# Performance work log

Measured on AMD Instinct MI355X. Metric: run time of the kernel, lower is better.

## Reference

```python
import jax, jax.numpy as jnp
import numpy as np

B, S, D = 2, 2048, 1024
H = 16
HD = D // H


def setup_inputs() -> dict:
    key = jax.random.key(0)
    ks = jax.random.split(key, 6)
    x = jax.random.normal(ks[0], (B, S, D), dtype=jnp.float32)
    scale = 1.0 / np.sqrt(D)
    Wq = jax.random.normal(ks[1], (D, D), dtype=jnp.float32) * scale
    Wk = jax.random.normal(ks[2], (D, D), dtype=jnp.float32) * scale
    Wv = jax.random.normal(ks[3], (D, D), dtype=jnp.float32) * scale
    Wo = jax.random.normal(ks[4], (D, D), dtype=jnp.float32) * scale
    bo = jax.random.normal(ks[5], (D,), dtype=jnp.float32) * 0.01
    return {"x": x, "Wq": Wq, "Wk": Wk, "Wv": Wv, "Wo": Wo, "bo": bo}


def reference(x, Wq, Wk, Wv, Wo, bo):
    b, t, _ = x.shape
    # QKV projections (no bias), split into heads: [b, h, t, hd]
    q = (x @ Wq).reshape(b, t, H, HD).transpose(0, 2, 1, 3)
    k = (x @ Wk).reshape(b, t, H, HD).transpose(0, 2, 1, 3)
    v = (x @ Wv).reshape(b, t, H, HD).transpose(0, 2, 1, 3)
    # scores [b, h, t, t]; causal mask (upper triangle -> -inf) applied before scaling
    scores = jnp.einsum("bhqd,bhkd->bhqk", q, k)
    causal = jnp.triu(jnp.ones((t, t), dtype=bool), k=1)
    scores = jnp.where(causal, -jnp.inf, scores)
    attn = jax.nn.softmax(scores / jnp.sqrt(jnp.asarray(HD, scores.dtype)), axis=-1)
    ctx = jnp.einsum("bhqk,bhkd->bhqd", attn, v)
    ctx = ctx.transpose(0, 2, 1, 3).reshape(b, t, H * HD)
    return ctx @ Wo + bo
```

## Files before the change

### kernel.cpp

```cpp
#include <hip/hip_runtime.h>

#define B_ 2
#define S_ 2048
#define D_ 1024
#define H_ 16
#define HD_ 64
#define M_ (B_*S_)

typedef __attribute__((ext_vector_type(8))) short bf16x8;
typedef __attribute__((ext_vector_type(4))) short s16x4;
typedef __attribute__((ext_vector_type(4))) float f32x4;
typedef __attribute__((ext_vector_type(4))) unsigned int u32x4;

static __device__ __forceinline__ unsigned short f2bf(float f) {
  unsigned int u = __builtin_bit_cast(unsigned int, f);
  u += 0x7FFFu + ((u >> 16) & 1u);
  return (unsigned short)(u >> 16);
}

static __device__ __forceinline__ unsigned int cvt_pk_bf16(float a, float b) {
  unsigned int r;
  asm("v_cvt_pk_bf16_f32 %0, %1, %2" : "=v"(r) : "v"(a), "v"(b));
  return r;
}

static __device__ __forceinline__ void gload_lds16(const void* g, void* l) {
  __builtin_amdgcn_global_load_lds(
      (const __attribute__((address_space(1))) unsigned int*)g,
      (__attribute__((address_space(3))) unsigned int*)l, 16, 0, 0);
}

__global__ __launch_bounds__(256) void xcvt_kernel(const float* __restrict__ x,
                                                   unsigned short* __restrict__ xb) {
  size_t i = ((size_t)blockIdx.x * 256 + threadIdx.x) * 8;
  float4 a = ((const float4*)(x + i))[0];
  float4 b = ((const float4*)(x + i))[1];
  bf16x8 w;
  w[0]=(short)f2bf(a.x); w[1]=(short)f2bf(a.y); w[2]=(short)f2bf(a.z); w[3]=(short)f2bf(a.w);
  w[4]=(short)f2bf(b.x); w[5]=(short)f2bf(b.y); w[6]=(short)f2bf(b.z); w[7]=(short)f2bf(b.w);
  *(bf16x8*)(xb + i) = w;
}

__global__ void wtrans_kernel(const float* __restrict__ Wq, const float* __restrict__ Wk,
                              const float* __restrict__ Wv, const float* __restrict__ Wo,
                              unsigned short* __restrict__ wt) {
  __shared__ float tile[32][33];
  const float* W = blockIdx.z==0 ? Wq : blockIdx.z==1 ? Wk : blockIdx.z==2 ? Wv : Wo;
  unsigned short* out = wt + (size_t)blockIdx.z * D_ * D_;
  int n0 = blockIdx.x*32, k0 = blockIdx.y*32;
  int tx = threadIdx.x, ty = threadIdx.y;
  #pragma unroll
  for (int i=0;i<4;i++) tile[ty+i*8][tx] = W[(size_t)(k0+ty+i*8)*D_ + n0+tx];
  __syncthreads();
  #pragma unroll
  for (int i=0;i<4;i++) out[(size_t)(n0+ty+i*8)*D_ + (k0+tx)] = f2bf(tile[tx][ty+i*8]);
}

#define GEMM_K_LOOP(Abase, Bbase)                                                     \
  for (int ks = 0; ks < 16; ++ks) {                                                   \
    const int k0 = ks * 64;                                                           \
    __syncthreads();                                                                  \
    _Pragma("unroll")                                                                 \
    for (int p = 0; p < 4; ++p) {                                                     \
      int c = p*256 + t;                                                              \
      int row = c >> 3, sl = (c & 7) ^ (row & 7);                                     \
      gload_lds16(Abase + (size_t)row*D_ + k0 + sl*8, &As[(p*256 + wid*64)*8]);       \
    }                                                                                 \
    _Pragma("unroll")                                                                 \
    for (int p = 0; p < 4; ++p) {                                                     \
      int c = p*256 + t;                                                              \
      int row = c >> 3, sl = (c & 7) ^ (row & 7);                                     \
      gload_lds16(Bbase + (size_t)row*D_ + k0 + sl*8, &Bs[(p*256 + wid*64)*8]);       \
    }                                                                                 \
    __syncthreads();                                                                  \
    _Pragma("unroll")                                                                 \
    for (int kk = 0; kk < 2; ++kk) {                                                  \
      bf16x8 af[4], bfr[4];                                                           \
      _Pragma("unroll")                                                               \
      for (int m = 0; m < 4; ++m) {                                                   \
        int row = wr + m*16 + l15;                                                    \
        af[m] = *(const bf16x8*)((const char*)As + row*128 + (((kk*4+lg)^(row&7))<<4)); \
      }                                                                               \
      _Pragma("unroll")                                                               \
      for (int n = 0; n < 4; ++n) {                                                   \
        int row = wc + n*16 + l15;                                                    \
        bfr[n] = *(const bf16x8*)((const char*)Bs + row*128 + (((kk*4+lg)^(row&7))<<4)); \
      }                                                                               \
      _Pragma("unroll")                                                               \
      for (int m = 0; m < 4; ++m)                                                     \
        _Pragma("unroll")                                                             \
        for (int n = 0; n < 4; ++n)                                                   \
          acc[m][n] = __builtin_amdgcn_mfma_f32_16x16x32_bf16(af[m], bfr[n], acc[m][n], 0,0,0); \
    }                                                                                 \
  }

__global__ __launch_bounds__(256,3) void gemm_qkv_kernel(
    const unsigned short* __restrict__ xb, const unsigned short* __restrict__ wt,
    unsigned short* __restrict__ Qo, unsigned short* __restrict__ Ko,
    unsigned short* __restrict__ Vto) {
  __shared__ __align__(16) unsigned short As[128*64];
  __shared__ __align__(16) unsigned short Bs[128*64];
  const int z = blockIdx.z;
  const int m0 = blockIdx.y*128, n0 = blockIdx.x*128;
  const int t = threadIdx.x, lane = t & 63, wid = t >> 6;
  const int wr = (wid>>1)*64, wc = (wid&1)*64;
  const int l15 = lane & 15, lg = lane >> 4;
  const unsigned short* Ab = xb + (size_t)m0 * D_;
  const unsigned short* Bb = wt + (size_t)z * D_ * D_ + (size_t)n0 * D_;

  f32x4 acc[4][4];
  #pragma unroll
  for (int m=0;m<4;m++)
    #pragma unroll
    for (int n=0;n<4;n++) acc[m][n] = f32x4{0.f,0.f,0.f,0.f};

  GEMM_K_LOOP(Ab, Bb)

  const float qscale = 0.18033688011112042f;
  #pragma unroll
  for (int m=0;m<4;m++) {
    #pragma unroll
    for (int n=0;n<4;n++) {
      #pragma unroll
      for (int r=0;r<4;r++) {
        int gm = m0 + wr + m*16 + lg*4 + r;
        int gn = n0 + wc + n*16 + l15;
        int b = gm >> 11, s = gm & (S_-1);
        int h = gn >> 6,  d = gn & 63;
        float av = acc[m][n][r];
        if (z==0) av *= qscale;
        unsigned short val = f2bf(av);
        if (z==0)      Qo[(((size_t)(b*H_+h))*S_ + s)*HD_ + d] = val;
        else if (z==1) Ko[(((size_t)(b*H_+h))*S_ + s)*HD_ + d] = val;
        else           Vto[(((size_t)(b*H_+h))*HD_ + d)*S_ + s] = val;
      }
    }
  }
}

__global__ __launch_bounds__(256,4) void attn_kernel(
    const unsigned short* __restrict__ Q, const unsigned short* __restrict__ K,
    const unsigned short* __restrict__ Vt, unsigned short* __restrict__ ctx) {
  __shared__ __align__(16) unsigned short KT[2][64*64];
  __shared__ __align__(16) unsigned short VT[2][64*64];
  __shared__ __align__(16) unsigned short PL[4][16*64];
  const int t = threadIdx.x, lane = t & 63, wid = t >> 6;
  const int bh = blockIdx.x & 31;
  const int qt = 31 - (int)(blockIdx.x >> 5);
  const int b = bh >> 4, h = bh & 15;
  const int q0 = qt * 64, qw0 = q0 + wid * 16;
  const int nchunk = qt + 1;
  const unsigned short* Qp = Q  + (size_t)bh * S_ * HD_;
  const unsigned short* Kp = K  + (size_t)bh * S_ * HD_;
  const unsigned short* Vp = Vt + (size_t)bh * HD_ * S_;
  const int l15 = lane & 15, lg = lane >> 4;
  const int rsub = lane >> 3, slot = lane & 7;
  const int sslot = slot ^ rsub;
  const int swp = (l15 & 7) << 4;

  bf16x8 qf0 = *(const bf16x8*)(Qp + (size_t)(qw0 + l15)*HD_ + lg*8);
  bf16x8 qf1 = *(const bf16x8*)(Qp + (size_t)(qw0 + l15)*HD_ + 32 + lg*8);

  f32x4 o[4];
  #pragma unroll
  for (int dt=0;dt<4;dt++) o[dt] = f32x4{0.f,0.f,0.f,0.f};
  float lsum = 0.f;

  auto stage = [&](int ch, int buf) {
    const int kk0 = ch * 64;
    #pragma unroll
    for (int j=0;j<2;j++) {
      int row = 16*wid + 8*j + rsub;
      gload_lds16(Kp + (size_t)(kk0 + row)*HD_ + sslot*8, &KT[buf][(16*wid + 8*j)*64]);
      gload_lds16(Vp + (size_t)row*S_ + kk0 + sslot*8,    &VT[buf][(16*wid + 8*j)*64]);
    }
  };

  stage(0, 0);
  __syncthreads();

  for (int ch=0; ch<nchunk; ++ch) {
    const int cur = ch & 1;
    const int kk0 = ch * 64;
    if (ch + 1 < nchunk) stage(ch+1, cur^1);

    const unsigned short* Kt = &KT[cur][0];
    const unsigned short* Vv = &VT[cur][0];

    f32x4 st[4];
    __builtin_amdgcn_s_setprio(1);
    #pragma unroll
    for (int kt=0; kt<4; ++kt) {
      int row = kt*16 + l15;
      int sw = (row & 7) << 4;
      bf16x8 kf0 = *(const bf16x8*)((const char*)Kt + row*128 + ((lg*16)      ^ sw));
      bf16x8 kf1 = *(const bf16x8*)((const char*)Kt + row*128 + ((64 + lg*16) ^ sw));
      f32x4 z = f32x4{0.f,0.f,0.f,0.f};
      z = __builtin_amdgcn_mfma_f32_16x16x32_bf16(kf0, qf0, z, 0,0,0);
      z = __builtin_amdgcn_mfma_f32_16x16x32_bf16(kf1, qf1, z, 0,0,0);
      st[kt] = z;
    }
    __builtin_amdgcn_s_setprio(0);

    if (ch == nchunk-1) {
      const int q = qw0 + l15;
      #pragma unroll
      for (int kt=0;kt<4;kt++)
        #pragma unroll
        for (int r=0;r<4;r++)
          if (kk0 + kt*16 + lg*4 + r > q) st[kt][r] = -INFINITY;
    }

    float rs = 0.f;
    #pragma unroll
    for (int kt=0;kt<4;kt++) {
      #pragma unroll
      for (int r=0;r<4;r++) {
        float p = exp2f(st[kt][r]);
        st[kt][r] = p;
        rs += p;
      }
      uint2 pk;
      pk.x = cvt_pk_bf16(st[kt][0], st[kt][1]);
      pk.y = cvt_pk_bf16(st[kt][2], st[kt][3]);
      *(uint2*)((char*)&PL[wid][0] + l15*128 + ((kt*32 + lg*8) ^ swp)) = pk;
    }
    rs += __shfl_xor(rs, 16);
    rs += __shfl_xor(rs, 32);
    lsum += rs;

    bf16x8 pf0 = *(const bf16x8*)((const char*)&PL[wid][0] + l15*128 + ((lg*16)      ^ swp));
    bf16x8 pf1 = *(const bf16x8*)((const char*)&PL[wid][0] + l15*128 + ((64 + lg*16) ^ swp));

    __builtin_amdgcn_s_setprio(1);
    #pragma unroll
    for (int dt=0;dt<4;dt++) {
      int row = dt*16 + l15;
      int sw = (row & 7) << 4;
      bf16x8 vf0 = *(const bf16x8*)((const char*)Vv + row*128 + ((lg*16)      ^ sw));
      bf16x8 vf1 = *(const bf16x8*)((const char*)Vv + row*128 + ((64 + lg*16) ^ sw));
      o[dt] = __builtin_amdgcn_mfma_f32_16x16x32_bf16(pf0, vf0, o[dt], 0,0,0);
      o[dt] = __builtin_amdgcn_mfma_f32_16x16x32_bf16(pf1, vf1, o[dt], 0,0,0);
    }
    __builtin_amdgcn_s_setprio(0);

    __syncthreads();
  }

  float li = 1.f / lsum;
  float lr[4];
  #pragma unroll
  for (int r=0;r<4;r++) lr[r] = __shfl(li, lg*4 + r);
  #pragma unroll
  for (int dt=0;dt<4;dt++)
    #pragma unroll
    for (int r=0;r<4;r++) {
      size_t row = (size_t)(b*S_ + qw0 + lg*4 + r);
      ctx[row*D_ + h*HD_ + dt*16 + l15] = f2bf(o[dt][r] * lr[r]);
    }
}

__global__ __launch_bounds__(256,3) void gemm_out_kernel(
    const unsigned short* __restrict__ ctx, const unsigned short* __restrict__ WtO,
    const float* __restrict__ bo, float* __restrict__ out) {
  __shared__ __align__(16) unsigned short As[128*64];
  __shared__ __align__(16) unsigned short Bs[128*64];
  const int m0 = blockIdx.y*128, n0 = blockIdx.x*128;
  const int t = threadIdx.x, lane = t & 63, wid = t >> 6;
  const int wr = (wid>>1)*64, wc = (wid&1)*64;
  const int l15 = lane & 15, lg = lane >> 4;
  const unsigned short* Ab = ctx + (size_t)m0 * D_;
  const unsigned short* Bb = WtO + (size_t)n0 * D_;

  f32x4 acc[4][4];
  #pragma unroll
  for (int m=0;m<4;m++)
    #pragma unroll
    for (int n=0;n<4;n++) acc[m][n] = f32x4{0.f,0.f,0.f,0.f};

  GEMM_K_LOOP(Ab, Bb)

  #pragma unroll
  for (int n=0;n<4;n++) {
    float bias = bo[n0 + wc + n*16 + l15];
    #pragma unroll
    for (int m=0;m<4;m++)
      #pragma unroll
      for (int r=0;r<4;r++) {
        int gm = m0 + wr + m*16 + lg*4 + r;
        int gn = n0 + wc + n*16 + l15;
        out[(size_t)gm*D_ + gn] = acc[m][n][r] + bias;
      }
  }
}

extern "C" void kernel_launch(void* const* d_in, const int* in_sizes, int n_in,
                              void* d_out, int out_size, void* d_ws, size_t ws_size,
                              hipStream_t stream) {
  (void)in_sizes; (void)n_in; (void)out_size; (void)ws_size;
  const float* x  = (const float*)d_in[0];
  const float* Wq = (const float*)d_in[1];
  const float* Wk = (const float*)d_in[2];
  const float* Wv = (const float*)d_in[3];
  const float* Wo = (const float*)d_in[4];
  const float* bo = (const float*)d_in[5];
  float* out = (float*)d_out;

  unsigned short* wt  = (unsigned short*)d_ws;
  unsigned short* Qb  = wt  + (size_t)4*D_*D_;
  unsigned short* Kb  = Qb  + (size_t)M_*D_;
  unsigned short* Vtb = Kb  + (size_t)M_*D_;
  unsigned short* ctb = Vtb + (size_t)M_*D_;
  unsigned short* xbb = ctb + (size_t)M_*D_;

  xcvt_kernel<<<dim3(M_*D_/(256*8)), 256, 0, stream>>>(x, xbb);
  wtrans_kernel<<<dim3(32,32,4), dim3(32,8), 0, stream>>>(Wq, Wk, Wv, Wo, wt);
  gemm_qkv_kernel<<<dim3(8,32,3), 256, 0, stream>>>(xbb, wt, Qb, Kb, Vtb);
  attn_kernel<<<dim3(1024), 256, 0, stream>>>(Qb, Kb, Vtb, ctb);
  gemm_out_kernel<<<dim3(8,32), 256, 0, stream>>>(ctb, wt + (size_t)3*D_*D_, bo, out);
}
```

Baseline: 113.9 us.

## Keep P in registers and use 16x16x16 MFMA for PV, dropping LDS round-trip

The softmax probabilities are no longer written to and reread from a per-wave LDS buffer. Each lane's S-tile accumulator layout is fed directly as the A operand of 16x16x16 bf16 MFMAs, which double the PV MFMA instruction count while halving per-instruction K. The row-sum cross-lane shuffle reduction moves out of the chunk loop to run once at the end. This removes LDS stores, loads and per-chunk shuffles, at the cost of more, smaller MFMAs and more 8-byte V reads from LDS.

```diff
diff --git a/kernel.cpp b/kernel.cpp
--- a/kernel.cpp
+++ b/kernel.cpp
@@ -143,7 +143,6 @@
     const unsigned short* __restrict__ Vt, unsigned short* __restrict__ ctx) {
   __shared__ __align__(16) unsigned short KT[2][64*64];
   __shared__ __align__(16) unsigned short VT[2][64*64];
-  __shared__ __align__(16) unsigned short PL[4][16*64];
   const int t = threadIdx.x, lane = t & 63, wid = t >> 6;
   const int bh = blockIdx.x & 31;
   const int qt = 31 - (int)(blockIdx.x >> 5);
@@ -156,7 +155,6 @@
   const int l15 = lane & 15, lg = lane >> 4;
   const int rsub = lane >> 3, slot = lane & 7;
   const int sslot = slot ^ rsub;
-  const int swp = (l15 & 7) << 4;
 
   bf16x8 qf0 = *(const bf16x8*)(Qp + (size_t)(qw0 + l15)*HD_ + lg*8);
   bf16x8 qf1 = *(const bf16x8*)(Qp + (size_t)(qw0 + l15)*HD_ + 32 + lg*8);
@@ -184,8 +182,8 @@
     const int kk0 = ch * 64;
     if (ch + 1 < nchunk) stage(ch+1, cur^1);
 
-    const unsigned short* Kt = &KT[cur][0];
-    const unsigned short* Vv = &VT[cur][0];
+    const char* Kt = (const char*)&KT[cur][0];
+    const char* Vv = (const char*)&VT[cur][0];
 
     f32x4 st[4];
     __builtin_amdgcn_s_setprio(1);
@@ -193,8 +191,8 @@
     for (int kt=0; kt<4; ++kt) {
       int row = kt*16 + l15;
       int sw = (row & 7) << 4;
-      bf16x8 kf0 = *(const bf16x8*)((const char*)Kt + row*128 + ((lg*16)      ^ sw));
-      bf16x8 kf1 = *(const bf16x8*)((const char*)Kt + row*128 + ((64 + lg*16) ^ sw));
+      bf16x8 kf0 = *(const bf16x8*)(Kt + row*128 + ((lg*16)      ^ sw));
+      bf16x8 kf1 = *(const bf16x8*)(Kt + row*128 + ((64 + lg*16) ^ sw));
       f32x4 z = f32x4{0.f,0.f,0.f,0.f};
       z = __builtin_amdgcn_mfma_f32_16x16x32_bf16(kf0, qf0, z, 0,0,0);
       z = __builtin_amdgcn_mfma_f32_16x16x32_bf16(kf1, qf1, z, 0,0,0);
@@ -211,42 +209,40 @@
           if (kk0 + kt*16 + lg*4 + r > q) st[kt][r] = -INFINITY;
     }
 
-    float rs = 0.f;
+    s16x4 pa[4];
     #pragma unroll
     for (int kt=0;kt<4;kt++) {
       #pragma unroll
       for (int r=0;r<4;r++) {
         float p = exp2f(st[kt][r]);
         st[kt][r] = p;
-        rs += p;
+        lsum += p;
       }
-      uint2 pk;
-      pk.x = cvt_pk_bf16(st[kt][0], st[kt][1]);
-      pk.y = cvt_pk_bf16(st[kt][2], st[kt][3]);
-      *(uint2*)((char*)&PL[wid][0] + l15*128 + ((kt*32 + lg*8) ^ swp)) = pk;
-    }
-    rs += __shfl_xor(rs, 16);
-    rs += __shfl_xor(rs, 32);
-    lsum += rs;
-
-    bf16x8 pf0 = *(const bf16x8*)((const char*)&PL[wid][0] + l15*128 + ((lg*16)      ^ swp));
-    bf16x8 pf1 = *(const bf16x8*)((const char*)&PL[wid][0] + l15*128 + ((64 + lg*16) ^ swp));
+      unsigned int plo = cvt_pk_bf16(st[kt][0], st[kt][1]);
+      unsigned int phi = cvt_pk_bf16(st[kt][2], st[kt][3]);
+      uint2 u; u.x = plo; u.y = phi;
+      pa[kt] = __builtin_bit_cast(s16x4, u);
+    }
 
     __builtin_amdgcn_s_setprio(1);
     #pragma unroll
     for (int dt=0;dt<4;dt++) {
       int row = dt*16 + l15;
       int sw = (row & 7) << 4;
-      bf16x8 vf0 = *(const bf16x8*)((const char*)Vv + row*128 + ((lg*16)      ^ sw));
-      bf16x8 vf1 = *(const bf16x8*)((const char*)Vv + row*128 + ((64 + lg*16) ^ sw));
-      o[dt] = __builtin_amdgcn_mfma_f32_16x16x32_bf16(pf0, vf0, o[dt], 0,0,0);
-      o[dt] = __builtin_amdgcn_mfma_f32_16x16x32_bf16(pf1, vf1, o[dt], 0,0,0);
+      const char* vrow = Vv + row*128;
+      #pragma unroll
+      for (int kt=0;kt<4;kt++) {
+        s16x4 vb = *(const s16x4*)(vrow + ((kt*32 + lg*8) ^ sw));
+        o[dt] = __builtin_amdgcn_mfma_f32_16x16x16bf16_1k(pa[kt], vb, o[dt], 0,0,0);
+      }
     }
     __builtin_amdgcn_s_setprio(0);
 
     __syncthreads();
   }
 
+  lsum += __shfl_xor(lsum, 16);
+  lsum += __shfl_xor(lsum, 32);
   float li = 1.f / lsum;
   float lr[4];
   #pragma unroll
```

Result: no change. 113.5 us (-0.4%).
